# Kernel tuning notes

Hardware: AMD Instinct MI355X
Metric: run time of the kernel (lower is better)

The kernel has to match this reference:

```python
import jax, jax.numpy as jnp
import numpy as np


def setup_inputs() -> dict:
    key = jax.random.key(0)
    k1, k2 = jax.random.split(key)
    x = jax.random.normal(k1, (8, 64, 256, 256), dtype=jnp.float32)
    gamma = jax.random.normal(k2, (1,), dtype=jnp.float32)
    return {"x": x, "gamma": gamma}


def reference(x, gamma):
    # NOTE: the torch code does `proj_query -= avg` in-place on a view of x,
    # so proj_value (another view of x) is ALSO mean-centered. We replicate that.
    B, C, H, W = x.shape
    n = H * W
    q = x.reshape(B, C, n)
    q = q - jnp.mean(q, axis=2, keepdims=True)  # centered channels, [B,C,N]
    # energy[b,c,d] = (1/n) * sum_n q[b,c,n]*q[b,d,n]  -> [B,C,C] covariance
    energy = jnp.einsum('bcn,bdn->bcd', q, q) / n
    attention = jax.nn.softmax(energy, axis=-1)
    out = jnp.einsum('bcd,bdn->bcn', attention, q).reshape(B, C, H, W)
    return gamma * out
```

## Files before the change

kernel.cpp:

```cpp
#include <hip/hip_runtime.h>
#include <hip/hip_bf16.h>

typedef __attribute__((ext_vector_type(8))) short short8;
typedef __attribute__((ext_vector_type(4))) short short4v;
typedef __attribute__((ext_vector_type(4))) float f32x4;
typedef __attribute__((ext_vector_type(8))) __bf16 bf16x8;

#define BB 8
#define CC 64
#define NN 65536
#define SPLIT1 64
#define COLS1 (NN / SPLIT1)
#define TILE_C 128
#define NT1 (COLS1 / TILE_C)
#define SPLIT3 128

__device__ inline short f2bf(float f) {
    __hip_bfloat16 h = __float2bfloat16(f);
    return __builtin_bit_cast(short, h);
}

template <typename V>
__device__ inline auto mfma_bf16_impl(V a, V b, f32x4 c, int)
    -> decltype(__builtin_amdgcn_mfma_f32_16x16x32_bf16(a, b, c, 0, 0, 0)) {
    return __builtin_amdgcn_mfma_f32_16x16x32_bf16(a, b, c, 0, 0, 0);
}
template <typename V>
__device__ inline f32x4 mfma_bf16_impl(V a, V b, f32x4 c, long) {
    bf16x8 a2 = __builtin_bit_cast(bf16x8, a);
    bf16x8 b2 = __builtin_bit_cast(bf16x8, b);
    return __builtin_amdgcn_mfma_f32_16x16x32_bf16(a2, b2, c, 0, 0, 0);
}
__device__ inline f32x4 mfma16(short8 a, short8 b, f32x4 c) {
    return mfma_bf16_impl(a, b, c, 0);
}

__device__ inline void stage_tile(const float* __restrict__ xb, int colbase,
                                  float* buf, int tid) {
    const int half = tid >> 5;
    const int sl   = tid & 31;
#pragma unroll
    for (int i = 0; i < 8; ++i) {
        const int row   = i * 8 + half;
        const int gbyte = (sl * 16) ^ ((row & 31) << 4);
        const float* gp = xb + (size_t)row * NN + colbase + (gbyte >> 2);
        float* lp = buf + i * 1024 + tid * 4;
#if __has_builtin(__builtin_amdgcn_global_load_lds)
        __builtin_amdgcn_global_load_lds(
            (const __attribute__((address_space(1))) void*)gp,
            (__attribute__((address_space(3))) void*)lp, 16, 0, 0);
#else
        *reinterpret_cast<f32x4*>(lp) = *reinterpret_cast<const f32x4*>(gp);
#endif
    }
}

__device__ inline void lds_read8(const float* buf, int row, int c0, float* v) {
    const char* rb = (const char*)(buf + row * TILE_C);
    const int swz = (row & 31) << 4;
    const f32x4 u0 = *reinterpret_cast<const f32x4*>(rb + ((c0 * 4) ^ swz));
    const f32x4 u1 = *reinterpret_cast<const f32x4*>(rb + (((c0 * 4) + 16) ^ swz));
    v[0] = u0[0]; v[1] = u0[1]; v[2] = u0[2]; v[3] = u0[3];
    v[4] = u1[0]; v[5] = u1[1]; v[6] = u1[2]; v[7] = u1[3];
}

__device__ inline short8 cvt8(const float* v) {
    short8 r;
#pragma unroll
    for (int j = 0; j < 8; ++j) r[j] = f2bf(v[j]);
    return r;
}

__global__ __launch_bounds__(256) void k1_gram(const float* __restrict__ x,
                                               float* __restrict__ partialG,
                                               float* __restrict__ partialS) {
    __shared__ float lbuf[2][CC * TILE_C];
    const int blk  = blockIdx.x;
    const int b    = blk / SPLIT1;
    const int s    = blk % SPLIT1;
    const int tid  = threadIdx.x;
    const int w    = tid >> 6, lane = tid & 63, lg = lane >> 4, lr = lane & 15;
    const float* xb = x + (size_t)b * CC * NN;
    const int colbase0 = s * COLS1;

    f32x4 acc[4];
#pragma unroll
    for (int dt = 0; dt < 4; ++dt) acc[dt] = (f32x4){0.f, 0.f, 0.f, 0.f};
    float asum = 0.f;

    stage_tile(xb, colbase0, lbuf[0], tid);
    __syncthreads();

    for (int t = 0; t < NT1; ++t) {
        if (t + 1 < NT1)
            stage_tile(xb, colbase0 + (t + 1) * TILE_C, lbuf[(t + 1) & 1], tid);
        const float* buf = lbuf[t & 1];
#pragma unroll
        for (int kk = 0; kk < TILE_C / 32; ++kk) {
            const int c0 = kk * 32 + lg * 8;
            float av[8];
            lds_read8(buf, w * 16 + lr, c0, av);
#pragma unroll
            for (int j = 0; j < 8; ++j) asum += av[j];
            const short8 af = cvt8(av);
#pragma unroll
            for (int dt = 0; dt < 4; ++dt) {
                float bv[8];
                lds_read8(buf, dt * 16 + lr, c0, bv);
                const short8 bf = cvt8(bv);
                acc[dt] = mfma16(af, bf, acc[dt]);
            }
        }
        __syncthreads();
    }
#pragma unroll
    for (int dt = 0; dt < 4; ++dt) {
#pragma unroll
        for (int r = 0; r < 4; ++r) {
            const int c = w * 16 + lg * 4 + r;
            const int d = dt * 16 + lr;
            partialG[(size_t)blk * 4096 + c * 64 + d] = acc[dt][r];
        }
    }
    float v = asum;
    v += __shfl_xor(v, 16);
    v += __shfl_xor(v, 32);
    if (lg == 0) partialS[blk * CC + w * 16 + lr] = v;
}

__global__ __launch_bounds__(256) void k2a_reduceG(const float* __restrict__ partialG,
                                                   float* __restrict__ Gsum) {
    const int gid = blockIdx.x * 256 + threadIdx.x;
    const int b = gid >> 12;
    const int e = gid & 4095;
    float s = 0.f;
    for (int sp = 0; sp < SPLIT1; ++sp)
        s += partialG[(((size_t)(b * SPLIT1 + sp)) << 12) + e];
    Gsum[gid] = s;
}

__global__ __launch_bounds__(256) void k2b_softmax(const float* __restrict__ partialS,
                                                   const float* __restrict__ Gsum,
                                                   unsigned short* __restrict__ att,
                                                   float* __restrict__ offs) {
    __shared__ float mu[CC];
    __shared__ float ener[CC * CC];
    const int b = blockIdx.x;
    const int tid = threadIdx.x;
    if (tid < CC) {
        float s = 0.f;
        for (int sp = 0; sp < SPLIT1; ++sp) s += partialS[(b * SPLIT1 + sp) * CC + tid];
        mu[tid] = s * (1.f / NN);
    }
    __syncthreads();
    const float inv_n = 1.f / NN;
#pragma unroll
    for (int k = 0; k < 16; ++k) {
        const int e = tid + k * 256;
        const int c = e >> 6, d = e & 63;
        ener[e] = Gsum[(b << 12) + e] * inv_n - mu[c] * mu[d];
    }
    __syncthreads();
    const int w = tid >> 6, lane = tid & 63;
    for (int i = 0; i < 16; ++i) {
        const int c = w * 16 + i;
        const float v = ener[c * 64 + lane];
        float m = v;
        for (int off = 32; off > 0; off >>= 1) m = fmaxf(m, __shfl_xor(m, off));
        const float ev = __expf(v - m);
        float sum = ev;
        for (int off = 32; off > 0; off >>= 1) sum += __shfl_xor(sum, off);
        const float a = ev / sum;
        att[(b << 12) + c * 64 + lane] = (unsigned short)f2bf(a);
        float o = a * mu[lane];
        for (int off = 32; off > 0; off >>= 1) o += __shfl_xor(o, off);
        if (lane == 0) offs[b * CC + c] = o;
    }
}

__global__ __launch_bounds__(256) void k3_apply(const float* __restrict__ x,
                                                const unsigned short* __restrict__ att,
                                                const float* __restrict__ offs,
                                                const float* __restrict__ gamma,
                                                float* __restrict__ out) {
    const int blk  = blockIdx.x;
    const int b    = blk / SPLIT3;
    const int s    = blk % SPLIT3;
    const int tid  = threadIdx.x;
    const int w    = tid >> 6, lane = tid & 63, lg = lane >> 4, lr = lane & 15;
    const float g  = gamma[0];

    short8 afr[4][2];
#pragma unroll
    for (int ct = 0; ct < 4; ++ct)
#pragma unroll
        for (int ks = 0; ks < 2; ++ks)
            afr[ct][ks] = *reinterpret_cast<const short8*>(
                att + (((size_t)b) << 12) + (ct * 16 + lr) * 64 + ks * 32 + lg * 8);

    float offv[4][4];
#pragma unroll
    for (int ct = 0; ct < 4; ++ct)
#pragma unroll
        for (int r = 0; r < 4; ++r)
            offv[ct][r] = offs[b * CC + ct * 16 + lg * 4 + r];

    const int colblock = s * (NN / SPLIT3);
    const int GROUPS = (NN / SPLIT3) / (4 * 64);
    for (int itg = 0; itg < GROUPS; ++itg) {
        const int n0 = colblock + (w * GROUPS + itg) * 64;
        f32x4 acc[4][4];
#pragma unroll
        for (int ph = 0; ph < 4; ++ph)
#pragma unroll
            for (int ct = 0; ct < 4; ++ct) acc[ph][ct] = (f32x4){0.f, 0.f, 0.f, 0.f};

#pragma unroll
        for (int ks = 0; ks < 2; ++ks) {
            short8 bfr[4];
            const int d0 = ks * 32 + lg * 8;
            const float* xp = x + ((size_t)(b * CC + d0)) * NN + n0 + lr * 4;
#pragma unroll
            for (int j = 0; j < 8; ++j) {
                const float4 v = *reinterpret_cast<const float4*>(xp + (size_t)j * NN);
                bfr[0][j] = f2bf(v.x);
                bfr[1][j] = f2bf(v.y);
                bfr[2][j] = f2bf(v.z);
                bfr[3][j] = f2bf(v.w);
            }
#pragma unroll
            for (int ct = 0; ct < 4; ++ct) {
#pragma unroll
                for (int ph = 0; ph < 4; ++ph)
                    acc[ph][ct] = mfma16(afr[ct][ks], bfr[ph], acc[ph][ct]);
            }
        }
#pragma unroll
        for (int ct = 0; ct < 4; ++ct) {
#pragma unroll
            for (int r = 0; r < 4; ++r) {
                const int c = ct * 16 + lg * 4 + r;
                const float o = offv[ct][r];
                f32x4 vs;
                vs[0] = g * (acc[0][ct][r] - o);
                vs[1] = g * (acc[1][ct][r] - o);
                vs[2] = g * (acc[2][ct][r] - o);
                vs[3] = g * (acc[3][ct][r] - o);
                __builtin_nontemporal_store(
                    vs, reinterpret_cast<f32x4*>(out + ((size_t)(b * CC + c)) * NN + n0 + lr * 4));
            }
        }
    }
}

extern "C" void kernel_launch(void* const* d_in, const int* in_sizes, int n_in,
                              void* d_out, int out_size, void* d_ws, size_t ws_size,
                              hipStream_t stream) {
    const float* x     = (const float*)d_in[0];
    const float* gamma = (const float*)d_in[1];
    float* out = (float*)d_out;

    float* partialG = out;
    float* partialS = out + (size_t)BB * SPLIT1 * 4096;
    float* Gsum     = partialS + BB * SPLIT1 * CC;
    float* offs     = (float*)d_ws;
    unsigned short* att = (unsigned short*)((char*)d_ws + 4096);

    k1_gram<<<BB * SPLIT1, 256, 0, stream>>>(x, partialG, partialS);
    k2a_reduceG<<<(BB * 4096) / 256, 256, 0, stream>>>(partialG, Gsum);
    k2b_softmax<<<BB, 256, 0, stream>>>(partialS, Gsum, att, offs);
    k3_apply<<<BB * SPLIT3, 256, 0, stream>>>(x, att, offs, gamma, out);
}
```

Measured before the change: 84.24 us.

## Fuse Gram reduction and softmax into gram kernel via last-block atomic counter

The separate partial-Gram reduction and softmax kernels are removed. Each gram block now bumps a per-batch atomic counter, and the last block to finish for a batch reduces all partials and computes the softmax, attention and offsets in place. This removes two kernel launches and the Gsum round trip through memory, at the cost of an added memset launch, threadfences, and serial reduction work done by a single block per batch.

```diff
diff --git a/kernel.cpp b/kernel.cpp
--- a/kernel.cpp
+++ b/kernel.cpp
@@ -45,13 +45,9 @@
         const int gbyte = (sl * 16) ^ ((row & 31) << 4);
         const float* gp = xb + (size_t)row * NN + colbase + (gbyte >> 2);
         float* lp = buf + i * 1024 + tid * 4;
-#if __has_builtin(__builtin_amdgcn_global_load_lds)
         __builtin_amdgcn_global_load_lds(
             (const __attribute__((address_space(1))) void*)gp,
             (__attribute__((address_space(3))) void*)lp, 16, 0, 0);
-#else
-        *reinterpret_cast<f32x4*>(lp) = *reinterpret_cast<const f32x4*>(gp);
-#endif
     }
 }
 
@@ -71,10 +67,14 @@
     return r;
 }
 
-__global__ __launch_bounds__(256) void k1_gram(const float* __restrict__ x,
-                                               float* __restrict__ partialG,
-                                               float* __restrict__ partialS) {
-    __shared__ float lbuf[2][CC * TILE_C];
+__global__ __launch_bounds__(256) void k1_gram_fused(const float* __restrict__ x,
+                                                     float* __restrict__ partialG,
+                                                     float* __restrict__ partialS,
+                                                     int* __restrict__ counters,
+                                                     unsigned short* __restrict__ att,
+                                                     float* __restrict__ offs) {
+    __shared__ float shm[2 * CC * TILE_C];
+    __shared__ int is_last;
     const int blk  = blockIdx.x;
     const int b    = blk / SPLIT1;
     const int s    = blk % SPLIT1;
@@ -82,19 +82,22 @@
     const int w    = tid >> 6, lane = tid & 63, lg = lane >> 4, lr = lane & 15;
     const float* xb = x + (size_t)b * CC * NN;
     const int colbase0 = s * COLS1;
+    float* lbuf0 = shm;
+    float* lbuf1 = shm + CC * TILE_C;
 
     f32x4 acc[4];
 #pragma unroll
     for (int dt = 0; dt < 4; ++dt) acc[dt] = (f32x4){0.f, 0.f, 0.f, 0.f};
     float asum = 0.f;
 
-    stage_tile(xb, colbase0, lbuf[0], tid);
+    stage_tile(xb, colbase0, lbuf0, tid);
     __syncthreads();
 
     for (int t = 0; t < NT1; ++t) {
         if (t + 1 < NT1)
-            stage_tile(xb, colbase0 + (t + 1) * TILE_C, lbuf[(t + 1) & 1], tid);
-        const float* buf = lbuf[t & 1];
+            stage_tile(xb, colbase0 + (t + 1) * TILE_C,
+                       ((t + 1) & 1) ? lbuf1 : lbuf0, tid);
+        const float* buf = (t & 1) ? lbuf1 : lbuf0;
 #pragma unroll
         for (int kk = 0; kk < TILE_C / 32; ++kk) {
             const int c0 = kk * 32 + lg * 8;
@@ -126,48 +129,46 @@
     v += __shfl_xor(v, 16);
     v += __shfl_xor(v, 32);
     if (lg == 0) partialS[blk * CC + w * 16 + lr] = v;
-}
-
-__global__ __launch_bounds__(256) void k2a_reduceG(const float* __restrict__ partialG,
-                                                   float* __restrict__ Gsum) {
-    const int gid = blockIdx.x * 256 + threadIdx.x;
-    const int b = gid >> 12;
-    const int e = gid & 4095;
-    float s = 0.f;
-    for (int sp = 0; sp < SPLIT1; ++sp)
-        s += partialG[(((size_t)(b * SPLIT1 + sp)) << 12) + e];
-    Gsum[gid] = s;
-}
-
-__global__ __launch_bounds__(256) void k2b_softmax(const float* __restrict__ partialS,
-                                                   const float* __restrict__ Gsum,
-                                                   unsigned short* __restrict__ att,
-                                                   float* __restrict__ offs) {
-    __shared__ float mu[CC];
-    __shared__ float ener[CC * CC];
-    const int b = blockIdx.x;
-    const int tid = threadIdx.x;
+
+    __threadfence();
+    __syncthreads();
+    if (tid == 0)
+        is_last = (atomicAdd(&counters[b], 1) == SPLIT1 - 1);
+    __syncthreads();
+    if (!is_last) return;
+    __threadfence();
+
+    float* mu   = shm;
+    float* ener = shm + 64;
     if (tid < CC) {
-        float s = 0.f;
-        for (int sp = 0; sp < SPLIT1; ++sp) s += partialS[(b * SPLIT1 + sp) * CC + tid];
-        mu[tid] = s * (1.f / NN);
-    }
-    __syncthreads();
+        float ssum = 0.f;
+        for (int sp = 0; sp < SPLIT1; ++sp)
+            ssum += partialS[(b * SPLIT1 + sp) * CC + tid];
+        mu[tid] = ssum * (1.f / NN);
+    }
+    f32x4 sg[4];
+#pragma unroll
+    for (int p = 0; p < 4; ++p) sg[p] = (f32x4){0.f, 0.f, 0.f, 0.f};
+    for (int sp = 0; sp < SPLIT1; ++sp) {
+        const f32x4* base = reinterpret_cast<const f32x4*>(
+            partialG + (((size_t)(b * SPLIT1 + sp)) << 12));
+#pragma unroll
+        for (int p = 0; p < 4; ++p) sg[p] += base[p * 256 + tid];
+    }
     const float inv_n = 1.f / NN;
 #pragma unroll
-    for (int k = 0; k < 16; ++k) {
-        const int e = tid + k * 256;
-        const int c = e >> 6, d = e & 63;
-        ener[e] = Gsum[(b << 12) + e] * inv_n - mu[c] * mu[d];
-    }
-    __syncthreads();
-    const int w = tid >> 6, lane = tid & 63;
+    for (int p = 0; p < 4; ++p) {
+        f32x4 e = sg[p];
+        e[0] *= inv_n; e[1] *= inv_n; e[2] *= inv_n; e[3] *= inv_n;
+        *reinterpret_cast<f32x4*>(&ener[(p * 256 + tid) * 4]) = e;
+    }
+    __syncthreads();
     for (int i = 0; i < 16; ++i) {
         const int c = w * 16 + i;
-        const float v = ener[c * 64 + lane];
-        float m = v;
+        const float e = ener[c * 64 + lane] - mu[c] * mu[lane];
+        float m = e;
         for (int off = 32; off > 0; off >>= 1) m = fmaxf(m, __shfl_xor(m, off));
-        const float ev = __expf(v - m);
+        const float ev = __expf(e - m);
         float sum = ev;
         for (int off = 32; off > 0; off >>= 1) sum += __shfl_xor(sum, off);
         const float a = ev / sum;
@@ -262,12 +263,12 @@
 
     float* partialG = out;
     float* partialS = out + (size_t)BB * SPLIT1 * 4096;
-    float* Gsum     = partialS + BB * SPLIT1 * CC;
-    float* offs     = (float*)d_ws;
+    int*   counters = (int*)d_ws;
+    float* offs     = (float*)((char*)d_ws + 1024);
     unsigned short* att = (unsigned short*)((char*)d_ws + 4096);
 
-    k1_gram<<<BB * SPLIT1, 256, 0, stream>>>(x, partialG, partialS);
-    k2a_reduceG<<<(BB * 4096) / 256, 256, 0, stream>>>(partialG, Gsum);
-    k2b_softmax<<<BB, 256, 0, stream>>>(partialS, Gsum, att, offs);
+    hipMemsetAsync(counters, 0, BB * sizeof(int), stream);
+    k1_gram_fused<<<BB * SPLIT1, 256, 0, stream>>>(x, partialG, partialS,
+                                                   counters, att, offs);
     k3_apply<<<BB * SPLIT3, 256, 0, stream>>>(x, att, offs, gamma, out);
 }
```

After: 156.1 us. +85.3%, slower.
